# Kernel optimization log

Measured on AMD Instinct MI355X. Metric: run time of the kernel, lower is better.

The kernel has to match this reference:

```python
import jax, jax.numpy as jnp
import numpy as np

N_NODES = 200000
N_EDGES = 600000
FP = 128


def _gru_cell(x, h, wih, whh, bih, bhh):
    # torch.nn.GRUCell: gates ordered (r, z, n)
    gi = x @ wih.T + bih
    gh = h @ whh.T + bhh
    ir, iz, inn = jnp.split(gi, 3, axis=-1)
    hr, hz, hn = jnp.split(gh, 3, axis=-1)
    r = jax.nn.sigmoid(ir + hr)
    z = jax.nn.sigmoid(iz + hz)
    n = jnp.tanh(inn + r * hn)
    return (1.0 - z) * n + z * h


def _layer(x, dst, step, aw, ab, tw, tb, wih, whh, bih, bhh):
    n_nodes = x.shape[0]
    x_i = x[dst]  # [E, F] gather of target-node features
    if step == 0:
        h_s = jnp.broadcast_to(jnp.sum(x_i, axis=-1, keepdims=True), x_i.shape)
    else:
        h_s = x_i
    esv = jax.nn.leaky_relu(jnp.concatenate([h_s, x_i], axis=-1) @ aw.T + ab)  # [E,1]
    asv = jax.nn.softmax(esv, axis=-1)  # size-1 softmax -> ones (faithful)
    cs = jax.nn.elu(asv * (h_s @ tw.T + tb))  # dropout is identity at eval
    m = _gru_cell(cs, h_s, wih, whh, bih, bhh)  # per-edge GRU update [E,F]
    return jax.ops.segment_sum(m, dst, num_segments=n_nodes)  # scatter-add aggregate


def setup_inputs() -> dict:
    key = jax.random.key(0)
    ks = jax.random.split(key, 20)
    s = 1.0 / np.sqrt(FP)
    inp = {
        "x": jax.random.normal(ks[0], (N_NODES, FP), dtype=jnp.float32),
        "edge_index": jax.random.randint(ks[1], (2, N_EDGES), 0, N_NODES, dtype=jnp.int64),
    }
    i = 2
    for l in range(2):
        inp[f"align_w{l}"] = jax.random.uniform(ks[i], (1, 2 * FP), jnp.float32, -s, s); i += 1
        inp[f"align_b{l}"] = jax.random.uniform(ks[i], (1,), jnp.float32, -s, s); i += 1
        inp[f"attend_w{l}"] = jax.random.uniform(ks[i], (FP, FP), jnp.float32, -s, s); i += 1
        inp[f"attend_b{l}"] = jax.random.uniform(ks[i], (FP,), jnp.float32, -s, s); i += 1
        inp[f"wih{l}"] = jax.random.uniform(ks[i], (3 * FP, FP), jnp.float32, -s, s); i += 1
        inp[f"whh{l}"] = jax.random.uniform(ks[i], (3 * FP, FP), jnp.float32, -s, s); i += 1
        inp[f"bih{l}"] = jax.random.uniform(ks[i], (3 * FP,), jnp.float32, -s, s); i += 1
        inp[f"bhh{l}"] = jax.random.uniform(ks[i], (3 * FP,), jnp.float32, -s, s); i += 1
    return inp


def reference(x, edge_index,
              align_w0, align_b0, attend_w0, attend_b0, wih0, whh0, bih0, bhh0,
              align_w1, align_b1, attend_w1, attend_b1, wih1, whh1, bih1, bhh1):
    dst = edge_index[1]
    x = _layer(x, dst, 0, align_w0, align_b0, attend_w0, attend_b0, wih0, whh0, bih0, bhh0)
    x = _layer(x, dst, 1, align_w1, align_b1, attend_w1, attend_b1, wih1, whh1, bih1, bhh1)
    return x
```

## Files before the change

kernel.cpp:

```cpp
#include <hip/hip_runtime.h>
#include <cmath>

#define NN 200000
#define NE 600000

typedef __bf16 bf16x8 __attribute__((ext_vector_type(8)));
typedef float f32x16 __attribute__((ext_vector_type(16)));

#define LOG2E 1.44269504088896340736f
__device__ __forceinline__ float fexp2(float x) { return __builtin_amdgcn_exp2f(x); }
__device__ __forceinline__ float frcp(float x) { return __builtin_amdgcn_rcpf(x); }
__device__ __forceinline__ float sigm(float v) { return frcp(1.0f + fexp2(-LOG2E * v)); }
__device__ __forceinline__ float ftanh(float v) {
  float t = fexp2(-2.0f * LOG2E * fabsf(v));
  float r = (1.0f - t) * frcp(1.0f + t);
  return __builtin_copysignf(r, v);
}
__device__ __forceinline__ float eluf(float v) { return v > 0.0f ? v : fexp2(LOG2E * v) - 1.0f; }

__device__ __forceinline__ unsigned short bfr(float f) {
  unsigned u = __float_as_uint(f);
  u += 0x7FFFu + ((u >> 16) & 1u);
  return (unsigned short)(u >> 16);
}
__device__ __forceinline__ void bsplit(float v, unsigned short& hi, unsigned short& lo) {
  unsigned short h = bfr(v);
  float hf = __uint_as_float(((unsigned)h) << 16);
  hi = h;
  lo = bfr(v - hf);
}


__global__ __launch_bounds__(256) void hist_kernel(const int* __restrict__ dst,
                                                   int* __restrict__ deg) {
  int e = blockIdx.x * 256 + threadIdx.x;
  if (e < NE) atomicAdd(&deg[dst[e]], 1);
}

__global__ __launch_bounds__(256) void prep_kernel(const float* __restrict__ attw0,
                                                   const float* __restrict__ whh0,
                                                   float* __restrict__ rwt0,
                                                   float* __restrict__ rwh0) {
  int gw = blockIdx.x * 4 + (threadIdx.x >> 6);
  int lane = threadIdx.x & 63;
  const float* row = (gw < 128) ? (attw0 + (size_t)gw * 128)
                                : (whh0 + (size_t)(gw - 128) * 128);
  float2 v = ((const float2*)row)[lane];
  float a = v.x + v.y;
#pragma unroll
  for (int o = 1; o < 64; o <<= 1) a += __shfl_xor(a, o, 64);
  if (lane == 0) {
    if (gw < 128) rwt0[gw] = a;
    else rwh0[gw - 128] = a;
  }
}

__global__ __launch_bounds__(256) void pack_kernel(
    const float* __restrict__ wih0, const float* __restrict__ tw1,
    const float* __restrict__ wih1, const float* __restrict__ whh1,
    unsigned short* __restrict__ w0ph, unsigned short* __restrict__ w0pl,
    unsigned short* __restrict__ w1ph, unsigned short* __restrict__ w1pl,
    unsigned short* __restrict__ w2ph, unsigned short* __restrict__ w2pl) {
  int g = blockIdx.x * 256 + threadIdx.x;
  if (g >= 20480) return;
  unsigned short *PH, *PL;
  const float* row;
  int l;
  if (g < 6144) { l = g; PH = w0ph; PL = w0pl; }
  else if (g < 8192) { l = g - 6144; PH = w1ph; PL = w1pl; }
  else { l = g - 8192; PH = w2ph; PL = w2pl; }
  int lane = l & 63, ks = (l >> 6) & 7, nt = l >> 9;
  int n = nt * 32 + (lane & 31);
  int k0 = ks * 16 + (lane >> 5) * 8;
  if (g < 6144) row = wih0 + n * 128;
  else if (g < 8192) row = tw1 + n * 128;
  else row = (n < 384) ? wih1 + n * 128 : whh1 + (n - 384) * 128;
  unsigned uh[4], ul[4];
#pragma unroll
  for (int p = 0; p < 4; p++) {
    unsigned short ah, al, bh, bl;
    bsplit(row[k0 + 2 * p], ah, al);
    bsplit(row[k0 + 2 * p + 1], bh, bl);
    uh[p] = (unsigned)ah | ((unsigned)bh << 16);
    ul[p] = (unsigned)al | ((unsigned)bl << 16);
  }
  *(uint4*)&PH[l * 8] = make_uint4(uh[0], uh[1], uh[2], uh[3]);
  *(uint4*)&PL[l * 8] = make_uint4(ul[0], ul[1], ul[2], ul[3]);
}

#define MFMA3(accv, ah, al, bh, bl)                                          \
  accv = __builtin_amdgcn_mfma_f32_32x32x16_bf16(ah, bh, accv, 0, 0, 0);     \
  accv = __builtin_amdgcn_mfma_f32_32x32x16_bf16(ah, bl, accv, 0, 0, 0);     \
  accv = __builtin_amdgcn_mfma_f32_32x32x16_bf16(al, bh, accv, 0, 0, 0);

__global__ __launch_bounds__(512, 4) void fused_kernel(
    const float* __restrict__ x,
    const float* __restrict__ tb0, const float* __restrict__ tb1,
    const unsigned short* __restrict__ w0ph, const unsigned short* __restrict__ w0pl,
    const unsigned short* __restrict__ w1ph, const unsigned short* __restrict__ w1pl,
    const unsigned short* __restrict__ w2ph, const unsigned short* __restrict__ w2pl,
    const float* __restrict__ bih0, const float* __restrict__ bhh0,
    const float* __restrict__ rwt0, const float* __restrict__ rwh0,
    const float* __restrict__ bih1, const float* __restrict__ bhh1,
    const int* __restrict__ deg, float* __restrict__ out) {
  extern __shared__ unsigned short smem[];
  unsigned short* csh = smem;
  unsigned short* csl = smem + 8192;
  unsigned short* hfh = smem + 16384;
  unsigned short* hfl = smem + 24576;
  __shared__ float s_lds[64];
  __shared__ float deg_lds[64];

  const int tid = threadIdx.x;
  const int lane = tid & 63;
  const int wv = tid >> 6;
  const int mg = wv & 1;
  const int cb = wv >> 1;
  const int n0 = blockIdx.x * 64;

  if (tid < 64) deg_lds[tid] = (float)deg[n0 + tid];

  {
    int m = tid >> 3, c = (tid & 7) * 16;
    const float4* xr = (const float4*)(x + (size_t)(n0 + m) * 128 + c);
    float a = 0.f;
#pragma unroll
    for (int q = 0; q < 4; q++) { float4 v = xr[q]; a += v.x + v.y + v.z + v.w; }
#pragma unroll
    for (int o = 1; o < 8; o <<= 1) a += __shfl_xor(a, o, 64);
    if ((tid & 7) == 0) s_lds[m] = a;
  }
  __syncthreads();

  {
    int m = lane, c = wv;
    float s = s_lds[m];
    int kb = c * 16;
    int fb = (((m >> 5) * 8 + c) * 64 + (m & 31)) * 8;
#pragma unroll
    for (int u = 0; u < 2; u++) {
      unsigned uh[4], ul[4];
#pragma unroll
      for (int p = 0; p < 4; p++) {
        int k = kb + u * 8 + p * 2;
        unsigned short h0, l0, h1, l1;
        bsplit(eluf(fmaf(s, rwt0[k], tb0[k])), h0, l0);
        bsplit(eluf(fmaf(s, rwt0[k + 1], tb0[k + 1])), h1, l1);
        uh[p] = (unsigned)h0 | ((unsigned)h1 << 16);
        ul[p] = (unsigned)l0 | ((unsigned)l1 << 16);
      }
      *(uint4*)&csh[fb + u * 256] = make_uint4(uh[0], uh[1], uh[2], uh[3]);
      *(uint4*)&csl[fb + u * 256] = make_uint4(ul[0], ul[1], ul[2], ul[3]);
    }
  }
  __syncthreads();

  const int jc = cb * 32 + (lane & 31);
  const int fj = ((mg * 8 + (cb * 2 + ((lane >> 4) & 1))) * 64 + ((lane >> 3) & 1) * 32) * 8 +
                 (lane & 7);

  f32x16 g0[3] = {};
#pragma unroll
  for (int ks = 0; ks < 8; ks++) {
    bf16x8 ah = *(const bf16x8*)&csh[((mg * 8 + ks) * 64 + lane) * 8];
    bf16x8 al = *(const bf16x8*)&csl[((mg * 8 + ks) * 64 + lane) * 8];
#pragma unroll
    for (int g = 0; g < 3; g++) {
      int nt = g * 4 + cb;
      size_t base = (size_t)((nt * 8 + ks) * 64 + lane) * 8;
      bf16x8 bh = *(const bf16x8*)&w0ph[base];
      bf16x8 bl = *(const bf16x8*)&w0pl[base];
      MFMA3(g0[g], ah, al, bh, bl);
    }
  }

  {
    float bir = bih0[jc], biz = bih0[jc + 128], bin_ = bih0[jc + 256];
    float bhr = bhh0[jc], bhz = bhh0[jc + 128], bhn = bhh0[jc + 256];
    float rwr = rwh0[jc], rwz = rwh0[jc + 128], rwn = rwh0[jc + 256];
#pragma unroll
    for (int reg = 0; reg < 16; reg++) {
      int crow = (reg & 3) + 8 * (reg >> 2) + 4 * (lane >> 5);
      int m = mg * 32 + crow;
      float s = s_lds[m];
      float dd = deg_lds[m];
      float r = sigm(g0[0][reg] + bir + fmaf(s, rwr, bhr));
      float z = sigm(g0[1][reg] + biz + fmaf(s, rwz, bhz));
      float nn2 = ftanh(fmaf(r, fmaf(s, rwn, bhn), g0[2][reg] + bin_));
      float v = dd * ((1.f - z) * nn2 + z * s);
      unsigned short vh, vl;
      bsplit(v, vh, vl);
      unsigned pv = (unsigned)vh | ((unsigned)vl << 16);
      unsigned pu = __shfl_xor(pv, 1, 64);
      if ((lane & 1) == 0) {
        int f = fj + crow * 8;
        *(unsigned*)&hfh[f] = (pv & 0xFFFFu) | (pu << 16);
        *(unsigned*)&hfl[f] = (pv >> 16) | (pu & 0xFFFF0000u);
      }
    }
  }
  __syncthreads();

  f32x16 a1 = {};
#pragma unroll
  for (int ks = 0; ks < 8; ks++) {
    bf16x8 ah = *(const bf16x8*)&hfh[((mg * 8 + ks) * 64 + lane) * 8];
    bf16x8 al = *(const bf16x8*)&hfl[((mg * 8 + ks) * 64 + lane) * 8];
    size_t base = (size_t)((cb * 8 + ks) * 64 + lane) * 8;
    bf16x8 bh = *(const bf16x8*)&w1ph[base];
    bf16x8 bl = *(const bf16x8*)&w1pl[base];
    MFMA3(a1, ah, al, bh, bl);
  }

  {
    float tbj = tb1[jc];
#pragma unroll
    for (int reg = 0; reg < 16; reg++) {
      int crow = (reg & 3) + 8 * (reg >> 2) + 4 * (lane >> 5);
      unsigned short vh, vl;
      bsplit(eluf(a1[reg] + tbj), vh, vl);
      unsigned pv = (unsigned)vh | ((unsigned)vl << 16);
      unsigned pu = __shfl_xor(pv, 1, 64);
      if ((lane & 1) == 0) {
        int f = fj + crow * 8;
        *(unsigned*)&csh[f] = (pv & 0xFFFFu) | (pu << 16);
        *(unsigned*)&csl[f] = (pv >> 16) | (pu & 0xFFFF0000u);
      }
    }
  }
  __syncthreads();

  f32x16 aR = {}, aZ = {}, aGHN = {}, aGIN = {};
#pragma unroll
  for (int ks = 0; ks < 8; ks++) {
    bf16x8 xh = *(const bf16x8*)&hfh[((mg * 8 + ks) * 64 + lane) * 8];
    bf16x8 xl = *(const bf16x8*)&hfl[((mg * 8 + ks) * 64 + lane) * 8];
    bf16x8 ch = *(const bf16x8*)&csh[((mg * 8 + ks) * 64 + lane) * 8];
    bf16x8 cl = *(const bf16x8*)&csl[((mg * 8 + ks) * 64 + lane) * 8];
#pragma unroll
    for (int g = 0; g < 3; g++) {
      {
        size_t base = (size_t)(((12 + g * 4 + cb) * 8 + ks) * 64 + lane) * 8;
        bf16x8 bh = *(const bf16x8*)&w2ph[base];
        bf16x8 bl = *(const bf16x8*)&w2pl[base];
        if (g == 0) { MFMA3(aR, xh, xl, bh, bl); }
        else if (g == 1) { MFMA3(aZ, xh, xl, bh, bl); }
        else { MFMA3(aGHN, xh, xl, bh, bl); }
      }
      {
        size_t base = (size_t)(((g * 4 + cb) * 8 + ks) * 64 + lane) * 8;
        bf16x8 bh = *(const bf16x8*)&w2ph[base];
        bf16x8 bl = *(const bf16x8*)&w2pl[base];
        if (g == 0) { MFMA3(aR, ch, cl, bh, bl); }
        else if (g == 1) { MFMA3(aZ, ch, cl, bh, bl); }
        else { MFMA3(aGIN, ch, cl, bh, bl); }
      }
    }
  }

  {
    float bir = bih1[jc], biz = bih1[jc + 128], bin_ = bih1[jc + 256];
    float bhr = bhh1[jc], bhz = bhh1[jc + 128], bhn = bhh1[jc + 256];
#pragma unroll
    for (int reg = 0; reg < 16; reg++) {
      int crow = (reg & 3) + 8 * (reg >> 2) + 4 * (lane >> 5);
      int m = mg * 32 + crow;
      float dd = deg_lds[m];
      float r = sigm(aR[reg] + bir + bhr);
      float z = sigm(aZ[reg] + biz + bhz);
      float nn2 = ftanh(fmaf(r, aGHN[reg] + bhn, aGIN[reg] + bin_));
      int f = fj + crow * 8;
      float hfull = (float)(*(const __bf16*)&hfh[f]) + (float)(*(const __bf16*)&hfl[f]);
      out[(size_t)(n0 + m) * 128 + jc] = dd * ((1.f - z) * nn2 + z * hfull);
    }
  }
}

extern "C" void kernel_launch(void* const* d_in, const int* in_sizes, int n_in,
                              void* d_out, int out_size, void* d_ws, size_t ws_size,
                              hipStream_t stream) {
  const float* x     = (const float*)d_in[0];
  const int*   edge  = (const int*)d_in[1];
  const float* attw0 = (const float*)d_in[4];
  const float* attb0 = (const float*)d_in[5];
  const float* wih0  = (const float*)d_in[6];
  const float* whh0  = (const float*)d_in[7];
  const float* bih0  = (const float*)d_in[8];
  const float* bhh0  = (const float*)d_in[9];
  const float* attw1 = (const float*)d_in[12];
  const float* attb1 = (const float*)d_in[13];
  const float* wih1  = (const float*)d_in[14];
  const float* whh1  = (const float*)d_in[15];
  const float* bih1  = (const float*)d_in[16];
  const float* bhh1  = (const float*)d_in[17];

  float* ws = (float*)d_ws;
  int*   deg  = (int*)(ws + 25600000);
  float* rwt0 = ws + 25800000;
  float* rwh0 = ws + 25800128;
  unsigned short* wp = (unsigned short*)(ws + 25800512);
  unsigned short* w0ph = wp;
  unsigned short* w0pl = wp + 49152;
  unsigned short* w1ph = wp + 98304;
  unsigned short* w1pl = wp + 114688;
  unsigned short* w2ph = wp + 131072;
  unsigned short* w2pl = wp + 229376;

  const int* dst = edge + NE;

  static bool attr_done = false;
  if (!attr_done) {
    hipFuncSetAttribute(reinterpret_cast<const void*>(fused_kernel),
                        hipFuncAttributeMaxDynamicSharedMemorySize, 65536);
    attr_done = true;
  }

  hipMemsetAsync(deg, 0, NN * sizeof(int), stream);
  hist_kernel<<<(NE + 255) / 256, 256, 0, stream>>>(dst, deg);
  prep_kernel<<<128, 256, 0, stream>>>(attw0, whh0, rwt0, rwh0);
  pack_kernel<<<80, 256, 0, stream>>>(wih0, attw1, wih1, whh1,
                                      w0ph, w0pl, w1ph, w1pl, w2ph, w2pl);
  fused_kernel<<<NN / 64, 512, 65536, stream>>>(
      x, attb0, attb1, w0ph, w0pl, w1ph, w1pl, w2ph, w2pl,
      bih0, bhh0, rwt0, rwh0, bih1, bhh1, deg, (float*)d_out);
}
```

Baseline: 450.4 us.

## Pad LDS fragment stride, merge prologue kernels, reorder layer-1 GEMMs

Merges the degree histogram, weight row-sum prep and weight packing into one launch to cut launch overhead. Pads the per-k-slice LDS fragment stride from 512 to 520 elements to reduce bank conflicts on the scattered h writes. Moves the hidden-state GRU matmuls of layer 1 into the loop that already reads hf, so hf fragments are loaded once. This keeps four accumulators live across the middle epilogue, which may raise register pressure, and LDS use grows slightly.

```diff
diff --git a/kernel.cpp b/kernel.cpp
--- a/kernel.cpp
+++ b/kernel.cpp
@@ -3,6 +3,7 @@
 
 #define NN 200000
 #define NE 600000
+#define FSTR 520
 
 typedef __bf16 bf16x8 __attribute__((ext_vector_type(8)));
 typedef float f32x16 __attribute__((ext_vector_type(16)));
@@ -31,37 +32,38 @@
 }
 
 
-__global__ __launch_bounds__(256) void hist_kernel(const int* __restrict__ dst,
-                                                   int* __restrict__ deg) {
-  int e = blockIdx.x * 256 + threadIdx.x;
-  if (e < NE) atomicAdd(&deg[dst[e]], 1);
-}
-
-__global__ __launch_bounds__(256) void prep_kernel(const float* __restrict__ attw0,
-                                                   const float* __restrict__ whh0,
-                                                   float* __restrict__ rwt0,
-                                                   float* __restrict__ rwh0) {
-  int gw = blockIdx.x * 4 + (threadIdx.x >> 6);
-  int lane = threadIdx.x & 63;
-  const float* row = (gw < 128) ? (attw0 + (size_t)gw * 128)
-                                : (whh0 + (size_t)(gw - 128) * 128);
-  float2 v = ((const float2*)row)[lane];
-  float a = v.x + v.y;
-#pragma unroll
-  for (int o = 1; o < 64; o <<= 1) a += __shfl_xor(a, o, 64);
-  if (lane == 0) {
-    if (gw < 128) rwt0[gw] = a;
-    else rwh0[gw - 128] = a;
-  }
-}
-
-__global__ __launch_bounds__(256) void pack_kernel(
+__global__ __launch_bounds__(256) void prologue_kernel(
+    const int* __restrict__ dst, int* __restrict__ deg,
+    const float* __restrict__ attw0, const float* __restrict__ whh0,
+    float* __restrict__ rwt0, float* __restrict__ rwh0,
     const float* __restrict__ wih0, const float* __restrict__ tw1,
-    const float* __restrict__ wih1, const float* __restrict__ whh1,
+    const float* __restrict__ wih1, const float* __restrict__ whh1f,
     unsigned short* __restrict__ w0ph, unsigned short* __restrict__ w0pl,
     unsigned short* __restrict__ w1ph, unsigned short* __restrict__ w1pl,
     unsigned short* __restrict__ w2ph, unsigned short* __restrict__ w2pl) {
-  int g = blockIdx.x * 256 + threadIdx.x;
+  const int bid = blockIdx.x;
+  const int tid = threadIdx.x;
+  if (bid < 2344) {
+    int e = bid * 256 + tid;
+    if (e < NE) atomicAdd(&deg[dst[e]], 1);
+    return;
+  }
+  if (bid < 2472) {
+    int gw = (bid - 2344) * 4 + (tid >> 6);
+    int lane = tid & 63;
+    const float* row = (gw < 128) ? (attw0 + (size_t)gw * 128)
+                                  : (whh0 + (size_t)(gw - 128) * 128);
+    float2 v = ((const float2*)row)[lane];
+    float a = v.x + v.y;
+#pragma unroll
+    for (int o = 1; o < 64; o <<= 1) a += __shfl_xor(a, o, 64);
+    if (lane == 0) {
+      if (gw < 128) rwt0[gw] = a;
+      else rwh0[gw - 128] = a;
+    }
+    return;
+  }
+  int g = (bid - 2472) * 256 + tid;
   if (g >= 20480) return;
   unsigned short *PH, *PL;
   const float* row;
@@ -74,7 +76,7 @@
   int k0 = ks * 16 + (lane >> 5) * 8;
   if (g < 6144) row = wih0 + n * 128;
   else if (g < 8192) row = tw1 + n * 128;
-  else row = (n < 384) ? wih1 + n * 128 : whh1 + (n - 384) * 128;
+  else row = (n < 384) ? wih1 + n * 128 : whh1f + (n - 384) * 128;
   unsigned uh[4], ul[4];
 #pragma unroll
   for (int p = 0; p < 4; p++) {
@@ -105,9 +107,9 @@
     const int* __restrict__ deg, float* __restrict__ out) {
   extern __shared__ unsigned short smem[];
   unsigned short* csh = smem;
-  unsigned short* csl = smem + 8192;
-  unsigned short* hfh = smem + 16384;
-  unsigned short* hfl = smem + 24576;
+  unsigned short* csl = smem + 8320;
+  unsigned short* hfh = smem + 16640;
+  unsigned short* hfl = smem + 24960;
   __shared__ float s_lds[64];
   __shared__ float deg_lds[64];
 
@@ -136,7 +138,7 @@
     int m = lane, c = wv;
     float s = s_lds[m];
     int kb = c * 16;
-    int fb = (((m >> 5) * 8 + c) * 64 + (m & 31)) * 8;
+    int fb = ((m >> 5) * 8 + c) * FSTR + (m & 31) * 8;
 #pragma unroll
     for (int u = 0; u < 2; u++) {
       unsigned uh[4], ul[4];
@@ -156,14 +158,14 @@
   __syncthreads();
 
   const int jc = cb * 32 + (lane & 31);
-  const int fj = ((mg * 8 + (cb * 2 + ((lane >> 4) & 1))) * 64 + ((lane >> 3) & 1) * 32) * 8 +
-                 (lane & 7);
+  const int sbase = (mg * 8 + cb * 2 + ((lane >> 4) & 1)) * FSTR +
+                    ((lane >> 3) & 1) * 256 + (lane & 7);
 
   f32x16 g0[3] = {};
 #pragma unroll
   for (int ks = 0; ks < 8; ks++) {
-    bf16x8 ah = *(const bf16x8*)&csh[((mg * 8 + ks) * 64 + lane) * 8];
-    bf16x8 al = *(const bf16x8*)&csl[((mg * 8 + ks) * 64 + lane) * 8];
+    bf16x8 ah = *(const bf16x8*)&csh[(mg * 8 + ks) * FSTR + lane * 8];
+    bf16x8 al = *(const bf16x8*)&csl[(mg * 8 + ks) * FSTR + lane * 8];
 #pragma unroll
     for (int g = 0; g < 3; g++) {
       int nt = g * 4 + cb;
@@ -193,7 +195,7 @@
       unsigned pv = (unsigned)vh | ((unsigned)vl << 16);
       unsigned pu = __shfl_xor(pv, 1, 64);
       if ((lane & 1) == 0) {
-        int f = fj + crow * 8;
+        int f = sbase + crow * 8;
         *(unsigned*)&hfh[f] = (pv & 0xFFFFu) | (pu << 16);
         *(unsigned*)&hfl[f] = (pv >> 16) | (pu & 0xFFFF0000u);
       }
@@ -201,15 +203,26 @@
   }
   __syncthreads();
 
-  f32x16 a1 = {};
+  f32x16 a1 = {}, aR = {}, aZ = {}, aGHN = {};
 #pragma unroll
   for (int ks = 0; ks < 8; ks++) {
-    bf16x8 ah = *(const bf16x8*)&hfh[((mg * 8 + ks) * 64 + lane) * 8];
-    bf16x8 al = *(const bf16x8*)&hfl[((mg * 8 + ks) * 64 + lane) * 8];
-    size_t base = (size_t)((cb * 8 + ks) * 64 + lane) * 8;
-    bf16x8 bh = *(const bf16x8*)&w1ph[base];
-    bf16x8 bl = *(const bf16x8*)&w1pl[base];
-    MFMA3(a1, ah, al, bh, bl);
+    bf16x8 xh = *(const bf16x8*)&hfh[(mg * 8 + ks) * FSTR + lane * 8];
+    bf16x8 xl = *(const bf16x8*)&hfl[(mg * 8 + ks) * FSTR + lane * 8];
+    {
+      size_t base = (size_t)((cb * 8 + ks) * 64 + lane) * 8;
+      bf16x8 bh = *(const bf16x8*)&w1ph[base];
+      bf16x8 bl = *(const bf16x8*)&w1pl[base];
+      MFMA3(a1, xh, xl, bh, bl);
+    }
+#pragma unroll
+    for (int g = 0; g < 3; g++) {
+      size_t base = (size_t)(((12 + g * 4 + cb) * 8 + ks) * 64 + lane) * 8;
+      bf16x8 bh = *(const bf16x8*)&w2ph[base];
+      bf16x8 bl = *(const bf16x8*)&w2pl[base];
+      if (g == 0) { MFMA3(aR, xh, xl, bh, bl); }
+      else if (g == 1) { MFMA3(aZ, xh, xl, bh, bl); }
+      else { MFMA3(aGHN, xh, xl, bh, bl); }
+    }
   }
 
   {
@@ -222,7 +235,7 @@
       unsigned pv = (unsigned)vh | ((unsigned)vl << 16);
       unsigned pu = __shfl_xor(pv, 1, 64);
       if ((lane & 1) == 0) {
-        int f = fj + crow * 8;
+        int f = sbase + crow * 8;
         *(unsigned*)&csh[f] = (pv & 0xFFFFu) | (pu << 16);
         *(unsigned*)&csl[f] = (pv >> 16) | (pu & 0xFFFF0000u);
       }
@@ -230,31 +243,19 @@
   }
   __syncthreads();
 
-  f32x16 aR = {}, aZ = {}, aGHN = {}, aGIN = {};
+  f32x16 aGIN = {};
 #pragma unroll
   for (int ks = 0; ks < 8; ks++) {
-    bf16x8 xh = *(const bf16x8*)&hfh[((mg * 8 + ks) * 64 + lane) * 8];
-    bf16x8 xl = *(const bf16x8*)&hfl[((mg * 8 + ks) * 64 + lane) * 8];
-    bf16x8 ch = *(const bf16x8*)&csh[((mg * 8 + ks) * 64 + lane) * 8];
-    bf16x8 cl = *(const bf16x8*)&csl[((mg * 8 + ks) * 64 + lane) * 8];
+    bf16x8 ch = *(const bf16x8*)&csh[(mg * 8 + ks) * FSTR + lane * 8];
+    bf16x8 cl = *(const bf16x8*)&csl[(mg * 8 + ks) * FSTR + lane * 8];
 #pragma unroll
     for (int g = 0; g < 3; g++) {
-      {
-        size_t base = (size_t)(((12 + g * 4 + cb) * 8 + ks) * 64 + lane) * 8;
-        bf16x8 bh = *(const bf16x8*)&w2ph[base];
-        bf16x8 bl = *(const bf16x8*)&w2pl[base];
-        if (g == 0) { MFMA3(aR, xh, xl, bh, bl); }
-        else if (g == 1) { MFMA3(aZ, xh, xl, bh, bl); }
-        else { MFMA3(aGHN, xh, xl, bh, bl); }
-      }
-      {
-        size_t base = (size_t)(((g * 4 + cb) * 8 + ks) * 64 + lane) * 8;
-        bf16x8 bh = *(const bf16x8*)&w2ph[base];
-        bf16x8 bl = *(const bf16x8*)&w2pl[base];
-        if (g == 0) { MFMA3(aR, ch, cl, bh, bl); }
-        else if (g == 1) { MFMA3(aZ, ch, cl, bh, bl); }
-        else { MFMA3(aGIN, ch, cl, bh, bl); }
-      }
+      size_t base = (size_t)(((g * 4 + cb) * 8 + ks) * 64 + lane) * 8;
+      bf16x8 bh = *(const bf16x8*)&w2ph[base];
+      bf16x8 bl = *(const bf16x8*)&w2pl[base];
+      if (g == 0) { MFMA3(aR, ch, cl, bh, bl); }
+      else if (g == 1) { MFMA3(aZ, ch, cl, bh, bl); }
+      else { MFMA3(aGIN, ch, cl, bh, bl); }
     }
   }
 
@@ -269,7 +270,7 @@
       float r = sigm(aR[reg] + bir + bhr);
       float z = sigm(aZ[reg] + biz + bhz);
       float nn2 = ftanh(fmaf(r, aGHN[reg] + bhn, aGIN[reg] + bin_));
-      int f = fj + crow * 8;
+      int f = sbase + crow * 8;
       float hfull = (float)(*(const __bf16*)&hfh[f]) + (float)(*(const __bf16*)&hfl[f]);
       out[(size_t)(n0 + m) * 128 + jc] = dd * ((1.f - z) * nn2 + z * hfull);
     }
@@ -311,16 +312,15 @@
   static bool attr_done = false;
   if (!attr_done) {
     hipFuncSetAttribute(reinterpret_cast<const void*>(fused_kernel),
-                        hipFuncAttributeMaxDynamicSharedMemorySize, 65536);
+                        hipFuncAttributeMaxDynamicSharedMemorySize, 66560);
     attr_done = true;
   }
 
   hipMemsetAsync(deg, 0, NN * sizeof(int), stream);
-  hist_kernel<<<(NE + 255) / 256, 256, 0, stream>>>(dst, deg);
-  prep_kernel<<<128, 256, 0, stream>>>(attw0, whh0, rwt0, rwh0);
-  pack_kernel<<<80, 256, 0, stream>>>(wih0, attw1, wih1, whh1,
-                                      w0ph, w0pl, w1ph, w1pl, w2ph, w2pl);
-  fused_kernel<<<NN / 64, 512, 65536, stream>>>(
+  prologue_kernel<<<2552, 256, 0, stream>>>(dst, deg, attw0, whh0, rwt0, rwh0,
+                                            wih0, attw1, wih1, whh1,
+                                            w0ph, w0pl, w1ph, w1pl, w2ph, w2pl);
+  fused_kernel<<<NN / 64, 512, 66560, stream>>>(
       x, attb0, attb1, w0ph, w0pl, w1ph, w1pl, w2ph, w2pl,
       bih0, bhh0, rwt0, rwh0, bih1, bhh1, deg, (float*)d_out);
 }
```

New measurement: 548.3 us. 1.22x slower.
